# Optimization experiments

Hardware: AMD Instinct MI355X
Metric: run time of the kernel (lower is better)

Reference implementation:

```python
import jax, jax.numpy as jnp
import numpy as np

B, S_IMG, S_TXT = 1, 3072, 512
D_MODEL, H, D_HEAD = 3072, 24, 128
INNER = H * D_HEAD
EPS = 1e-5


def rms_norm(x, w):
    # x: [..., D_HEAD]
    var = jnp.mean(jnp.square(x), axis=-1, keepdims=True)
    return x * jax.lax.rsqrt(var + EPS) * w


def apply_rope(x, cos, sin):
    # x: [B,S,H,D]; cos/sin: [S,D]; interleaved (non-neox) rotation
    x1 = x[..., 0::2]
    x2 = x[..., 1::2]
    rot = jnp.stack([-x2, x1], axis=-1).reshape(x.shape)
    c = cos[None, :, None, :]
    s = sin[None, :, None, :]
    return x * c + rot * s


def setup_inputs() -> dict:
    key = jax.random.key(0)
    ks = jax.random.split(key, 12)
    sc = 1.0 / np.sqrt(D_MODEL)
    ang = jax.random.uniform(ks[10], (S_TXT + S_IMG, D_HEAD), jnp.float32, 0.0, 2 * np.pi)
    return {
        "hidden_states": jax.random.normal(ks[0], (B, S_IMG, D_MODEL), jnp.float32),
        "encoder_hidden_states": jax.random.normal(ks[1], (B, S_TXT, D_MODEL), jnp.float32),
        "cos": jnp.cos(ang),
        "sin": jnp.sin(ang),
        "W_qkv": jax.random.normal(ks[2], (3 * INNER, D_MODEL), jnp.float32) * sc,
        "W_add_qkv": jax.random.normal(ks[3], (3 * INNER, D_MODEL), jnp.float32) * sc,
        "b_add_qkv": jnp.zeros((3 * INNER,), jnp.float32),
        "norm_q_w": jnp.ones((D_HEAD,), jnp.float32),
        "norm_k_w": jnp.ones((D_HEAD,), jnp.float32),
        "norm_add_q_w": jnp.ones((D_HEAD,), jnp.float32),
        "norm_add_k_w": jnp.ones((D_HEAD,), jnp.float32),
        "W_out": jax.random.normal(ks[4], (D_MODEL, INNER), jnp.float32) * sc,
        "b_out": jnp.zeros((D_MODEL,), jnp.float32),
        "W_add_out": jax.random.normal(ks[5], (D_MODEL, INNER), jnp.float32) * sc,
        "b_add_out": jnp.zeros((D_MODEL,), jnp.float32),
    }


def reference(hidden_states, encoder_hidden_states, cos, sin,
              W_qkv, W_add_qkv, b_add_qkv,
              norm_q_w, norm_k_w, norm_add_q_w, norm_add_k_w,
              W_out, b_out, W_add_out, b_add_out):
    # fused QKV projections
    qkv = jnp.einsum('bsd,ed->bse', hidden_states, W_qkv)
    q, k, v = jnp.split(qkv, 3, axis=-1)
    eqkv = jnp.einsum('bsd,ed->bse', encoder_hidden_states, W_add_qkv) + b_add_qkv
    eq, ek, ev = jnp.split(eqkv, 3, axis=-1)

    def heads(x):
        return x.reshape(x.shape[0], x.shape[1], H, D_HEAD)

    q, k, v = heads(q), heads(k), heads(v)
    eq, ek, ev = heads(eq), heads(ek), heads(ev)

    # per-head RMSNorm on queries/keys
    q = rms_norm(q, norm_q_w)
    k = rms_norm(k, norm_k_w)
    eq = rms_norm(eq, norm_add_q_w)
    ek = rms_norm(ek, norm_add_k_w)

    # joint concat: text first, then image
    q = jnp.concatenate([eq, q], axis=1)
    k = jnp.concatenate([ek, k], axis=1)
    v = jnp.concatenate([ev, v], axis=1)

    # RoPE on full joint sequence
    q = apply_rope(q, cos, sin)
    k = apply_rope(k, cos, sin)

    # non-causal softmax attention, scale = 1/sqrt(head_dim)
    scale = 1.0 / np.sqrt(D_HEAD)
    scores = jnp.einsum('bqhd,bkhd->bhqk', q, k) * scale
    probs = jax.nn.softmax(scores, axis=-1)
    out = jnp.einsum('bhqk,bkhd->bqhd', probs, v)  # [B,S,H,D]
    out = out.reshape(out.shape[0], out.shape[1], INNER)

    enc_out = out[:, :S_TXT]
    img_out = out[:, S_TXT:]
    enc_out = jnp.einsum('bse,de->bsd', enc_out, W_add_out) + b_add_out
    img_out = jnp.einsum('bse,de->bsd', img_out, W_out) + b_out
    return (img_out, enc_out)
```

## Files before the change

### kernel.cpp

```cpp
#include <hip/hip_runtime.h>


typedef unsigned short u16;
typedef __attribute__((ext_vector_type(2))) unsigned short u16x2;
typedef __attribute__((ext_vector_type(4))) unsigned short u16x4;
typedef __attribute__((ext_vector_type(8))) unsigned short u16x8;
typedef __attribute__((ext_vector_type(8))) short bf16x8;
typedef __attribute__((ext_vector_type(4))) float f32x4;
typedef __attribute__((ext_vector_type(16))) float f32x16;
typedef __attribute__((ext_vector_type(4))) unsigned u32x4;

#define DEV __device__ __forceinline__

DEV u16 f2bf(float f) {
  unsigned u = __builtin_bit_cast(unsigned, f);
  u = (u + 0x7FFFu + ((u >> 16) & 1u)) >> 16;
  return (u16)u;
}
DEV float bf2f(u16 s) { return __builtin_bit_cast(float, (unsigned)s << 16); }

DEV void store_out(u16* p, float v)  { *p = f2bf(v); }
DEV void store_out(float* p, float v) { *p = v; }

#define AS1(p) (const __attribute__((address_space(1))) void*)(p)
#define AS3(p) (__attribute__((address_space(3))) void*)(p)
#define GLL16(g, l) __builtin_amdgcn_global_load_lds(AS1(g), AS3(l), 16, 0, 0)

#define BAR() do { asm volatile("" ::: "memory"); __builtin_amdgcn_s_barrier(); \
                   asm volatile("" ::: "memory"); } while (0)
#define LGKM0() asm volatile("s_waitcnt lgkmcnt(0)" ::: "memory")
#define VMC8() asm volatile("s_waitcnt vmcnt(8)" ::: "memory")
#define VMC6() asm volatile("s_waitcnt vmcnt(6)" ::: "memory")
#define VMC0() asm volatile("s_waitcnt vmcnt(0)" ::: "memory")

__global__ __launch_bounds__(256) void cvt_all(
    const float* __restrict__ s0, const float* __restrict__ s1,
    const float* __restrict__ s2, const float* __restrict__ s3,
    const float* __restrict__ s4, const float* __restrict__ s5,
    u16* __restrict__ ws16) {
  constexpr int B1 = 393216, B2 = 2752512, B3 = 9830400,
                B4 = 16908288, B5 = 19267584, B6 = 21626880;
  int i = blockIdx.x * blockDim.x + threadIdx.x;
  int stride = gridDim.x * blockDim.x;
  for (; i < B6; i += stride) {
    const float* src; size_t off; u16* dst;
    if (i < B1)      { src = s0; off = i;      dst = ws16; }
    else if (i < B2) { src = s1; off = i - B1; dst = ws16 + 1572864; }
    else if (i < B3) { src = s2; off = i - B2; dst = ws16 + 11010048; }
    else if (i < B4) { src = s3; off = i - B3; dst = ws16 + 39321600; }
    else if (i < B5) { src = s4; off = i - B4; dst = ws16 + 67633152; }
    else             { src = s5; off = i - B5; dst = ws16 + 77070336; }
    float4 v = reinterpret_cast<const float4*>(src)[off];
    u16x4 o;
    o.x = f2bf(v.x); o.y = f2bf(v.y); o.z = f2bf(v.z); o.w = f2bf(v.w);
    reinterpret_cast<u16x4*>(dst)[off] = o;
  }
}

template <typename OT>
__global__ __launch_bounds__(512, 2) void gemm256(
    const u16* __restrict__ A,
    const u16* __restrict__ Bimg, const u16* __restrict__ Benc,
    const float* __restrict__ biasImg, const float* __restrict__ biasEnc,
    OT* __restrict__ Cimg, OT* __restrict__ Cenc,
    int N, int K, int split) {
  const int bid = blockIdx.x;
  const int ntn = N >> 8;
  const int CN = ntn >> 2;
  const int x = bid & 7, i5 = bid >> 3;
  const int mt = (x >> 2) * 7 + i5 / CN;
  const int nt = (x & 3) * CN + i5 % CN;
  const int m0 = mt << 8, n0 = nt << 8;
  const u16* B = (m0 < split) ? Benc : Bimg;
  const float* bias = (m0 < split) ? biasEnc : biasImg;

  __shared__ u16 lds[2][2][2][8192];

  const int tid = threadIdx.x, w = tid >> 6, lane = tid & 63;
  const int wm = w >> 2, wn = w & 3;
  const int q = lane & 15, hi = lane >> 4;
  const size_t ldb = (size_t)K * 2;

  f32x4 acc[8][4];
#pragma unroll
  for (int i = 0; i < 8; ++i)
#pragma unroll
    for (int j = 0; j < 4; ++j)
#pragma unroll
      for (int r = 0; r < 4; ++r) acc[i][j][r] = 0.f;

  auto STG_B = [&](int kt, int h) {
    const int d = kt & 1;
    char* dst = (char*)&lds[d][1][h][0] + w * 1024 + lane * 16;
#pragma unroll
    for (int g = 0; g < 2; ++g) {
      const int n = g * 8 + w;
      const char* src = (const char*)B + (size_t)(n0 + h * 128 + (n >> 1) * 16 + q) * ldb
                        + (size_t)kt * 128 + (n & 1) * 64 + hi * 16;
      GLL16(src, dst + g * 8192);
    }
  };
  auto STG_A = [&](int kt, int g) {
    const int d = kt & 1;
#pragma unroll
    for (int h = 0; h < 2; ++h) {
      const int n = g * 8 + w;
      const char* src = (const char*)A + (size_t)(m0 + h * 128 + (n >> 1) * 16 + q) * ldb
                        + (size_t)kt * 128 + (n & 1) * 64 + hi * 16;
      GLL16(src, (char*)&lds[d][0][h][0] + n * 1024 + lane * 16);
    }
  };
  auto LDA = [&](int d, int i, int ks) -> bf16x8 {
    return *(const bf16x8*)((const char*)&lds[d][0][wm][0] + (i * 2 + ks) * 1024 + lane * 16);
  };
  auto LDB = [&](int d, int j, int ks) -> bf16x8 {
    return *(const bf16x8*)((const char*)&lds[d][1][wn >> 1][0]
                            + (((wn & 1) * 4 + j) * 2 + ks) * 1024 + lane * 16);
  };

  bf16x8 bfr[4][2];
  auto PH = [&](int d, int ph, auto stageFn, int wmode) {
    if (ph == 0) {
#pragma unroll
      for (int j = 0; j < 4; ++j)
#pragma unroll
        for (int ks = 0; ks < 2; ++ks) bfr[j][ks] = LDB(d, j, ks);
    }
    bf16x8 af[2][2];
#pragma unroll
    for (int m = 0; m < 2; ++m)
#pragma unroll
      for (int ks = 0; ks < 2; ++ks) af[m][ks] = LDA(d, 2 * ph + m, ks);
    stageFn();
    BAR();
    LGKM0();
    __builtin_amdgcn_s_setprio(1);
#pragma unroll
    for (int m = 0; m < 2; ++m)
#pragma unroll
      for (int j = 0; j < 4; ++j)
#pragma unroll
        for (int ks = 0; ks < 2; ++ks)
          acc[2 * ph + m][j] = __builtin_amdgcn_mfma_f32_16x16x32_bf16(
              af[m][ks], bfr[j][ks], acc[2 * ph + m][j], 0, 0, 0);
    __builtin_amdgcn_s_setprio(0);
    if (wmode == 1)      VMC6();
    else if (wmode == 2) VMC0();
    BAR();
  };

  const int NT2 = K >> 7;
  STG_B(0, 0); STG_B(0, 1); STG_A(0, 0); STG_A(0, 1);
  STG_B(1, 0); STG_B(1, 1); STG_A(1, 0);
  VMC6();
  BAR();
  for (int t = 0; t < NT2; ++t) {
    const bool full = (t + 1 < NT2);
    const int w3 = full ? 1 : 2;
    PH(0, 0, [&] { STG_A(2 * t + 1, 1); }, 0);
    PH(0, 1, [&] { if (full) STG_B(2 * t + 2, 0); }, 0);
    PH(0, 2, [&] { if (full) STG_B(2 * t + 2, 1); }, 0);
    PH(0, 3, [&] { if (full) STG_A(2 * t + 2, 0); }, w3);
    PH(1, 0, [&] { if (full) STG_A(2 * t + 2, 1); }, 0);
    PH(1, 1, [&] { if (full) STG_B(2 * t + 3, 0); }, 0);
    PH(1, 2, [&] { if (full) STG_B(2 * t + 3, 1); }, 0);
    PH(1, 3, [&] { if (full) STG_A(2 * t + 3, 0); }, w3);
  }

#pragma unroll
  for (int i = 0; i < 8; ++i) {
    int rbase = m0 + wm * 128 + i * 16 + (hi << 2);
#pragma unroll
    for (int j = 0; j < 4; ++j) {
      int col = n0 + wn * 64 + j * 16 + q;
      float bv = bias ? bias[col] : 0.f;
#pragma unroll
      for (int r = 0; r < 4; ++r) {
        int row = rbase + r;
        float v = acc[i][j][r] + bv;
        if (row < split) store_out(&Cenc[(size_t)row * N + col], v);
        else             store_out(&Cimg[(size_t)(row - split) * N + col], v);
      }
    }
  }
}

__global__ __launch_bounds__(256) void norm_rope(
    u16* __restrict__ qkv, u16* __restrict__ vt,
    const float* __restrict__ cosT, const float* __restrict__ sinT,
    const float* __restrict__ nqw_img, const float* __restrict__ nkw_img,
    const float* __restrict__ nqw_enc, const float* __restrict__ nkw_enc) {
  const int h = blockIdx.y;
  const int s0 = blockIdx.x * 64;
  const int tid = threadIdx.x, w = tid >> 6, lane = tid & 63;
  const bool enc = (s0 < 512);
  const float* nqw = enc ? nqw_enc : nqw_img;
  const float* nkw = enc ? nkw_enc : nkw_img;
  const float SCL = 0.12751743f;
  const float wq0 = nqw[2 * lane], wq1 = nqw[2 * lane + 1];
  const float wk0 = nkw[2 * lane], wk1 = nkw[2 * lane + 1];
  u16x8 va0, va1, vb0, vb1;
#pragma unroll
  for (int r = 0; r < 16; ++r) {
    const int s = s0 + w * 16 + r;
    const size_t rowb = (size_t)s * 9216 + h * 128 + 2 * lane;
    float2 cv = *(const float2*)&cosT[(size_t)s * 128 + 2 * lane];
    float2 sv = *(const float2*)&sinT[(size_t)s * 128 + 2 * lane];
    {
      u16x2 qu = *(u16x2*)&qkv[rowb];
      float x0 = bf2f(qu.x), x1 = bf2f(qu.y);
      float ss = x0 * x0 + x1 * x1;
#pragma unroll
      for (int d = 1; d < 64; d <<= 1) ss += __shfl_xor(ss, d);
      float rms = rsqrtf(ss * (1.0f / 128.0f) + 1e-5f);
      x0 *= rms * wq0; x1 *= rms * wq1;
      float o0 = (x0 * cv.x - x1 * sv.x) * SCL;
      float o1 = (x1 * cv.y + x0 * sv.y) * SCL;
      u16x2 ou; ou.x = f2bf(o0); ou.y = f2bf(o1);
      *(u16x2*)&qkv[rowb] = ou;
    }
    {
      u16x2 ku = *(u16x2*)&qkv[rowb + 3072];
      float x0 = bf2f(ku.x), x1 = bf2f(ku.y);
      float ss = x0 * x0 + x1 * x1;
#pragma unroll
      for (int d = 1; d < 64; d <<= 1) ss += __shfl_xor(ss, d);
      float rms = rsqrtf(ss * (1.0f / 128.0f) + 1e-5f);
      x0 *= rms * wk0; x1 *= rms * wk1;
      float o0 = x0 * cv.x - x1 * sv.x;
      float o1 = x1 * cv.y + x0 * sv.y;
      u16x2 ou; ou.x = f2bf(o0); ou.y = f2bf(o1);
      *(u16x2*)&qkv[rowb + 3072] = ou;
    }
    {
      u16x2 vu = *(u16x2*)&qkv[rowb + 6144];
      if (r < 8) { va0[r] = vu.x; vb0[r] = vu.y; }
      else       { va1[r - 8] = vu.x; vb1[r - 8] = vu.y; }
    }
  }
  const size_t vbase = (size_t)h * 128 * 3584 + (size_t)(2 * lane) * 3584 + s0 + w * 16;
  *(u16x8*)&vt[vbase]            = va0;
  *(u16x8*)&vt[vbase + 8]        = va1;
  *(u16x8*)&vt[vbase + 3584]     = vb0;
  *(u16x8*)&vt[vbase + 3584 + 8] = vb1;
}

__global__ __launch_bounds__(256, 2) void attn_kernel(
    const u16* __restrict__ qkv, const u16* __restrict__ vt,
    u16* __restrict__ aout) {
  const int bid = blockIdx.x;
  const int qt = bid / 24;
  const int rr = bid % 24;
  const int h = (rr % 8) * 3 + (rr / 8);
  const int tid = threadIdx.x, w = tid >> 6, lane = tid & 63;
  const int q32 = lane & 31, hi5 = lane >> 5;
  const int qbase = qt * 128 + w * 32;
  __shared__ u16 Klds[3][4096];
  __shared__ u16 Vlds[3][4096];

  bf16x8 aq[8];
  {
    const u16* qp = qkv + (size_t)(qbase + q32) * 9216 + h * 128 + hi5 * 8;
#pragma unroll
    for (int ds = 0; ds < 8; ++ds) aq[ds] = *(const bf16x8*)(qp + ds * 16);
  }
  float m_i = -1e30f, l_i = 0.f;
  f32x16 o[4];
#pragma unroll
  for (int dt = 0; dt < 4; ++dt)
#pragma unroll
    for (int r = 0; r < 16; ++r) o[dt][r] = 0.f;
  const size_t vhead = (size_t)h * 128 * 3584;

  auto STAGE_K = [&](int kt0, int b) {
    const char* src = (const char*)(qkv + (size_t)(kt0 + q32) * 9216 + 3072 + h * 128) + hi5 * 16;
    char* dst = (char*)Klds[b] + w * 2048 + lane * 16;
#pragma unroll
    for (int j = 0; j < 2; ++j)
      GLL16(src + (w * 2 + j) * 32, dst + j * 1024);
  };
  auto STAGE_V = [&](int kt0, int b) {
    char* dst = (char*)Vlds[b] + w * 2048 + lane * 16;
#pragma unroll
    for (int j = 0; j < 2; ++j) {
      const int u = w * 2 + j, dt = u >> 1, ks = u & 1;
      GLL16((const char*)(vt + vhead + (size_t)(dt * 32 + q32) * 3584 + kt0) + ks * 32 + hi5 * 16,
            dst + j * 1024);
    }
  };

  auto PACK = [&](const float* p, bf16x8* out2) {
    unsigned w0[4], w1[4];
#pragma unroll
    for (int g = 0; g < 4; ++g) {
      asm("v_cvt_pk_bf16_f32 %0, %1, %2" : "=v"(w0[g]) : "v"(p[4 * g + 0]), "v"(p[4 * g + 1]));
      asm("v_cvt_pk_bf16_f32 %0, %1, %2" : "=v"(w1[g]) : "v"(p[4 * g + 2]), "v"(p[4 * g + 3]));
    }
    asm("v_permlane32_swap_b32 %0, %1" : "+v"(w0[0]), "+v"(w0[1]));
    asm("v_permlane32_swap_b32 %0, %1" : "+v"(w1[0]), "+v"(w1[1]));
    asm("v_permlane32_swap_b32 %0, %1" : "+v"(w0[2]), "+v"(w0[3]));
    asm("v_permlane32_swap_b32 %0, %1" : "+v"(w1[2]), "+v"(w1[3]));
    u32x4 lo = {w0[0], w1[0], w0[1], w1[1]};
    u32x4 hi_ = {w0[2], w1[2], w0[3], w1[3]};
    out2[0] = __builtin_bit_cast(bf16x8, lo);
    out2[1] = __builtin_bit_cast(bf16x8, hi_);
  };

  const int NT = 112;
  STAGE_K(0, 0);   STAGE_V(0, 0);
  STAGE_K(32, 1);  STAGE_V(32, 1);
  int cur = 0;
  for (int t = 0; t < NT; ++t) {
    if (t + 1 < NT) VMC8(); else VMC0();
    BAR();

    f32x16 sA, sB;
#pragma unroll
    for (int r = 0; r < 16; ++r) { sA[r] = 0.f; sB[r] = 0.f; }
    __builtin_amdgcn_s_setprio(1);
#pragma unroll
    for (int ds = 0; ds < 4; ++ds) {
      bf16x8 k0 = *(const bf16x8*)((const char*)Klds[cur] + ds * 1024 + lane * 16);
      bf16x8 k1 = *(const bf16x8*)((const char*)Klds[cur] + (ds + 4) * 1024 + lane * 16);
      sA = __builtin_amdgcn_mfma_f32_32x32x16_bf16(k0, aq[ds], sA, 0, 0, 0);
      sB = __builtin_amdgcn_mfma_f32_32x32x16_bf16(k1, aq[ds + 4], sB, 0, 0, 0);
    }
    __builtin_amdgcn_s_setprio(0);

    float v[16];
#pragma unroll
    for (int r = 0; r < 16; ++r) v[r] = sA[r] + sB[r];
    float m8[8], m4[4], m2[2];
#pragma unroll
    for (int i = 0; i < 8; ++i) m8[i] = fmaxf(v[2 * i], v[2 * i + 1]);
#pragma unroll
    for (int i = 0; i < 4; ++i) m4[i] = fmaxf(m8[2 * i], m8[2 * i + 1]);
    m2[0] = fmaxf(m4[0], m4[1]); m2[1] = fmaxf(m4[2], m4[3]);
    float mx = fmaxf(m2[0], m2[1]);
    mx = fmaxf(mx, __shfl_xor(mx, 32));
    if (!__all(mx - m_i <= 8.f)) {
      float mnew = fmaxf(m_i, mx);
      float alpha = __builtin_amdgcn_exp2f(m_i - mnew);
      m_i = mnew;
      l_i *= alpha;
#pragma unroll
      for (int r = 0; r < 16; ++r) {
        int qr = (r & 3) + 8 * (r >> 2) + 4 * hi5;
        float ar = __shfl(alpha, qr);
#pragma unroll
        for (int dt = 0; dt < 4; ++dt) o[dt][r] *= ar;
      }
    }
    float p0[16];
#pragma unroll
    for (int r = 0; r < 16; ++r) p0[r] = __builtin_amdgcn_exp2f(v[r] - m_i);
    float s8[8], s4[4], s2[2];
#pragma unroll
    for (int i = 0; i < 8; ++i) s8[i] = p0[2 * i] + p0[2 * i + 1];
#pragma unroll
    for (int i = 0; i < 4; ++i) s4[i] = s8[2 * i] + s8[2 * i + 1];
    s2[0] = s4[0] + s4[1]; s2[1] = s4[2] + s4[3];
    float psum = s2[0] + s2[1];
    psum += __shfl_xor(psum, 32);
    l_i += psum;

    bf16x8 pa[2];
    PACK(p0, pa);

    __builtin_amdgcn_s_setprio(1);
#pragma unroll
    for (int dt = 0; dt < 4; ++dt) {
#pragma unroll
      for (int ks = 0; ks < 2; ++ks) {
        bf16x8 bv = *(const bf16x8*)((const char*)Vlds[cur] + (dt * 2 + ks) * 1024 + lane * 16);
        o[dt] = __builtin_amdgcn_mfma_f32_32x32x16_bf16(pa[ks], bv, o[dt], 0, 0, 0);
      }
    }
    __builtin_amdgcn_s_setprio(0);

    if (t + 2 < NT) {
      const int stg = cur ? cur - 1 : 2;
      STAGE_K((t + 2) * 32, stg);
      STAGE_V((t + 2) * 32, stg);
    }
    cur = (cur == 2) ? 0 : cur + 1;
  }

#pragma unroll
  for (int r = 0; r < 16; ++r) {
    const int qr = (r & 3) + 8 * (r >> 2) + 4 * hi5;
    const float lr = __shfl(l_i, qr);
    const float inv = 1.0f / lr;
    const size_t srow = (size_t)(qbase + qr) * 3072 + h * 128 + q32;
#pragma unroll
    for (int dt = 0; dt < 4; ++dt)
      aout[srow + dt * 32] = f2bf(o[dt][r] * inv);
  }
}

extern "C" void kernel_launch(void* const* d_in, const int* in_sizes, int n_in,
                              void* d_out, int out_size, void* d_ws, size_t ws_size,
                              hipStream_t stream) {
  (void)in_sizes; (void)n_in; (void)out_size; (void)ws_size;
  const float* hs    = (const float*)d_in[0];
  const float* ehs   = (const float*)d_in[1];
  const float* cosT  = (const float*)d_in[2];
  const float* sinT  = (const float*)d_in[3];
  const float* Wqkv  = (const float*)d_in[4];
  const float* Wadd  = (const float*)d_in[5];
  const float* bAdd  = (const float*)d_in[6];
  const float* nqw   = (const float*)d_in[7];
  const float* nkw   = (const float*)d_in[8];
  const float* naqw  = (const float*)d_in[9];
  const float* nakw  = (const float*)d_in[10];
  const float* Wout  = (const float*)d_in[11];
  const float* bout  = (const float*)d_in[12];
  const float* Waddo = (const float*)d_in[13];
  const float* baddo = (const float*)d_in[14];

  char* ws = (char*)d_ws;
  u16* Ain = (u16*)(ws);
  u16* WqI = (u16*)(ws + 22020096);
  u16* WqE = WqI + (size_t)9216 * 3072;
  u16* WoI = (u16*)(ws + 135266304);
  u16* WoE = WoI + (size_t)3072 * 3072;
  u16* qkv = (u16*)(ws + 173015040);
  u16* vt   = Ain;
  u16* aout = WqI;

  cvt_all<<<4096, 256, 0, stream>>>(ehs, hs, Wqkv, Wadd, Wout, Waddo, (u16*)ws);

  gemm256<u16><<<dim3(504), 512, 0, stream>>>(Ain, WqI, WqE, nullptr, bAdd,
                                              qkv + (size_t)512 * 9216, qkv, 9216, 3072, 512);
  norm_rope<<<dim3(56, 24), 256, 0, stream>>>(qkv, vt, cosT, sinT, nqw, nkw, naqw, nakw);
  attn_kernel<<<dim3(672), 256, 0, stream>>>(qkv, vt, aout);
  float* outp = (float*)d_out;
  gemm256<float><<<dim3(168), 512, 0, stream>>>(aout, WoI, WoE, bout, baddo,
                                                outp, outp + (size_t)3072 * 3072, 3072, 3072, 512);
}
```

Before: 622.7 us.

## Use 256x192-tile GEMM for output projection to fill more CUs

Adds a new gemm192 kernel that tiles the output projection as 256x192 instead of 256x256, launching 224 blocks instead of 168 so the 256 CUs on the device are better covered. It keeps a phased double-buffered LDS pipeline with direct global-to-LDS loads, retuned for the narrower B tile, and uses a block-index swizzle across 8 groups. In exchange each block reuses A over fewer columns, and the new hand-tuned wait counts add some risk of pipeline stalls or ordering errors.

Result: slower. 643.4 us (+3.3%).

```diff
diff --git a/kernel.cpp b/kernel.cpp
--- a/kernel.cpp
+++ b/kernel.cpp
@@ -31,6 +31,7 @@
 #define LGKM0() asm volatile("s_waitcnt lgkmcnt(0)" ::: "memory")
 #define VMC8() asm volatile("s_waitcnt vmcnt(8)" ::: "memory")
 #define VMC6() asm volatile("s_waitcnt vmcnt(6)" ::: "memory")
+#define VMC5() asm volatile("s_waitcnt vmcnt(5)" ::: "memory")
 #define VMC0() asm volatile("s_waitcnt vmcnt(0)" ::: "memory")
 
 __global__ __launch_bounds__(256) void cvt_all(
@@ -185,6 +186,132 @@
   }
 }
 
+__global__ __launch_bounds__(512, 2) void gemm192(
+    const u16* __restrict__ A,
+    const u16* __restrict__ Bimg, const u16* __restrict__ Benc,
+    const float* __restrict__ biasImg, const float* __restrict__ biasEnc,
+    float* __restrict__ Cimg, float* __restrict__ Cenc,
+    int N, int K, int split) {
+  const int bid = blockIdx.x;
+  const int x = bid & 7, i5 = bid >> 3;
+  const int mt = (x >> 2) * 7 + i5 / 4;
+  const int nt = (x & 3) * 4 + i5 % 4;
+  const int m0 = mt << 8, n0 = nt * 192;
+  const u16* B = (m0 < split) ? Benc : Bimg;
+  const float* bias = (m0 < split) ? biasEnc : biasImg;
+
+  __shared__ u16 lds_a[2][2][8192];
+  __shared__ u16 lds_b[2][12288];
+
+  const int tid = threadIdx.x, w = tid >> 6, lane = tid & 63;
+  const int wm = w >> 2, wn = w & 3;
+  const int q = lane & 15, hi = lane >> 4;
+  const size_t ldb = (size_t)K * 2;
+
+  f32x4 acc[8][3];
+#pragma unroll
+  for (int i = 0; i < 8; ++i)
+#pragma unroll
+    for (int j = 0; j < 3; ++j)
+#pragma unroll
+      for (int r = 0; r < 4; ++r) acc[i][j][r] = 0.f;
+
+  auto STG_B3 = [&](int kt) {
+    const int d = kt & 1;
+    char* dst = (char*)&lds_b[d][0] + w * 1024 + lane * 16;
+#pragma unroll
+    for (int g = 0; g < 3; ++g) {
+      const int n = g * 8 + w;
+      const char* src = (const char*)B + (size_t)(n0 + (n >> 1) * 16 + q) * ldb
+                        + (size_t)kt * 128 + (n & 1) * 64 + hi * 16;
+      GLL16(src, dst + g * 8192);
+    }
+  };
+  auto STG_A = [&](int kt, int g) {
+    const int d = kt & 1;
+#pragma unroll
+    for (int h = 0; h < 2; ++h) {
+      const int n = g * 8 + w;
+      const char* src = (const char*)A + (size_t)(m0 + h * 128 + (n >> 1) * 16 + q) * ldb
+                        + (size_t)kt * 128 + (n & 1) * 64 + hi * 16;
+      GLL16(src, (char*)&lds_a[d][h][0] + n * 1024 + lane * 16);
+    }
+  };
+  auto LDA = [&](int d, int i, int ks) -> bf16x8 {
+    return *(const bf16x8*)((const char*)&lds_a[d][wm][0] + (i * 2 + ks) * 1024 + lane * 16);
+  };
+  auto LDB = [&](int d, int j, int ks) -> bf16x8 {
+    return *(const bf16x8*)((const char*)&lds_b[d][0]
+                            + ((wn * 3 + j) * 2 + ks) * 1024 + lane * 16);
+  };
+
+  bf16x8 bfr[3][2];
+  auto PH = [&](int d, int ph, auto stageFn, int wmode) {
+    if (ph == 0) {
+#pragma unroll
+      for (int j = 0; j < 3; ++j)
+#pragma unroll
+        for (int ks = 0; ks < 2; ++ks) bfr[j][ks] = LDB(d, j, ks);
+    }
+    bf16x8 af[2][2];
+#pragma unroll
+    for (int m = 0; m < 2; ++m)
+#pragma unroll
+      for (int ks = 0; ks < 2; ++ks) af[m][ks] = LDA(d, 2 * ph + m, ks);
+    stageFn();
+    BAR();
+    LGKM0();
+    __builtin_amdgcn_s_setprio(1);
+#pragma unroll
+    for (int m = 0; m < 2; ++m)
+#pragma unroll
+      for (int j = 0; j < 3; ++j)
+#pragma unroll
+        for (int ks = 0; ks < 2; ++ks)
+          acc[2 * ph + m][j] = __builtin_amdgcn_mfma_f32_16x16x32_bf16(
+              af[m][ks], bfr[j][ks], acc[2 * ph + m][j], 0, 0, 0);
+    __builtin_amdgcn_s_setprio(0);
+    if (wmode == 1)      VMC5();
+    else if (wmode == 2) VMC0();
+    BAR();
+  };
+
+  const int NT2 = K >> 7;
+  STG_B3(0); STG_A(0, 0); STG_A(0, 1);
+  STG_B3(1); STG_A(1, 0);
+  VMC5();
+  BAR();
+  for (int t = 0; t < NT2; ++t) {
+    const bool full = (t + 1 < NT2);
+    const int w3 = full ? 1 : 2;
+    PH(0, 0, [&] { STG_A(2 * t + 1, 1); }, 0);
+    PH(0, 1, [&] { if (full) STG_B3(2 * t + 2); }, 0);
+    PH(0, 2, [&] {}, 0);
+    PH(0, 3, [&] { if (full) STG_A(2 * t + 2, 0); }, w3);
+    PH(1, 0, [&] { if (full) STG_A(2 * t + 2, 1); }, 0);
+    PH(1, 1, [&] { if (full) STG_B3(2 * t + 3); }, 0);
+    PH(1, 2, [&] {}, 0);
+    PH(1, 3, [&] { if (full) STG_A(2 * t + 3, 0); }, w3);
+  }
+
+#pragma unroll
+  for (int i = 0; i < 8; ++i) {
+    int rbase = m0 + wm * 128 + i * 16 + (hi << 2);
+#pragma unroll
+    for (int j = 0; j < 3; ++j) {
+      int col = n0 + wn * 48 + j * 16 + q;
+      float bv = bias ? bias[col] : 0.f;
+#pragma unroll
+      for (int r = 0; r < 4; ++r) {
+        int row = rbase + r;
+        float v = acc[i][j][r] + bv;
+        if (row < split) Cenc[(size_t)row * N + col] = v;
+        else             Cimg[(size_t)(row - split) * N + col] = v;
+      }
+    }
+  }
+}
+
 __global__ __launch_bounds__(256) void norm_rope(
     u16* __restrict__ qkv, u16* __restrict__ vt,
     const float* __restrict__ cosT, const float* __restrict__ sinT,
@@ -435,6 +562,6 @@
   norm_rope<<<dim3(56, 24), 256, 0, stream>>>(qkv, vt, cosT, sinT, nqw, nkw, naqw, nakw);
   attn_kernel<<<dim3(672), 256, 0, stream>>>(qkv, vt, aout);
   float* outp = (float*)d_out;
-  gemm256<float><<<dim3(168), 512, 0, stream>>>(aout, WoI, WoE, bout, baddo,
-                                                outp, outp + (size_t)3072 * 3072, 3072, 3072, 512);
-}
+  gemm192<<<dim3(224), 512, 0, stream>>>(aout, WoI, WoE, bout, baddo,
+                                         outp, outp + (size_t)3072 * 3072, 3072, 3072, 512);
+}
```
